# Kernel optimization log

Hardware: AMD Instinct MI355X
Metric: run time of the kernel (lower is better)

The kernel has to match this reference:

```python
import jax, jax.numpy as jnp
import numpy as np

NUM_EVENT, EVENT_DIM = 6, 32
NUM_WORD, WORD_DIM = 100000, 128
NUM_SKU, SKU_DIM = 500000, 128
NUM_CAT, CAT_DIM = 10000, 64
NUM_PRICE, PRICE_DIM = 100, 32
NUM_URL, URL_DIM = 200000, 128
HIDDEN = 512
B, S, W = 256, 256, 12
PAD = 0


def _table(key, n, d):
    t = jax.random.normal(key, (n, d), dtype=jnp.float32) * 0.02
    return t.at[PAD].set(0.0)  # padding_idx row is zero


def setup_inputs() -> dict:
    key = jax.random.key(0)
    ks = jax.random.split(key, 20)
    inp = {
        "event_table": _table(ks[0], NUM_EVENT, EVENT_DIM),
        "word_table": _table(ks[1], NUM_WORD, WORD_DIM),
        "sku_table": _table(ks[2], NUM_SKU, SKU_DIM),
        "cat_table": _table(ks[3], NUM_CAT, CAT_DIM),
        "price_table": _table(ks[4], NUM_PRICE, PRICE_DIM),
        "url_table": _table(ks[5], NUM_URL, URL_DIM),
        # Linear weights, torch convention: y = x @ W.T + b
        "sku_w": jax.random.normal(ks[6], (HIDDEN, EVENT_DIM + SKU_DIM + CAT_DIM + PRICE_DIM + WORD_DIM), dtype=jnp.float32) * 0.02,
        "sku_b": jnp.zeros((HIDDEN,), dtype=jnp.float32),
        "url_w": jax.random.normal(ks[7], (HIDDEN, URL_DIM + EVENT_DIM), dtype=jnp.float32) * 0.02,
        "url_b": jnp.zeros((HIDDEN,), dtype=jnp.float32),
        "query_w": jax.random.normal(ks[8], (HIDDEN, EVENT_DIM + WORD_DIM), dtype=jnp.float32) * 0.02,
        "query_b": jnp.zeros((HIDDEN,), dtype=jnp.float32),
        "event_type": jax.random.randint(ks[9], (B, S), 0, NUM_EVENT, dtype=jnp.int32),
        "sku_id": jax.random.randint(ks[10], (B, S), 0, NUM_SKU, dtype=jnp.int32),
        "url_id": jax.random.randint(ks[11], (B, S), 0, NUM_URL, dtype=jnp.int32),
        "cat_id": jax.random.randint(ks[12], (B, S), 0, NUM_CAT, dtype=jnp.int32),
        "price_id": jax.random.randint(ks[13], (B, S), 0, NUM_PRICE, dtype=jnp.int32),
        "word_id": jax.random.randint(ks[14], (B, S, W), 0, NUM_WORD, dtype=jnp.int32),
    }
    return inp


def _linear_relu(x, w, b):
    return jax.nn.relu(jnp.einsum("bsi,hi->bsh", x, w) + b)


def reference(event_table, word_table, sku_table, cat_table, price_table, url_table,
              sku_w, sku_b, url_w, url_b, query_w, query_b,
              event_type, sku_id, url_id, cat_id, price_id, word_id):
    # padding mask: 1.0 where event_type == PAD_IDX
    src_padding_mask = (event_type == PAD).astype(jnp.float32)

    event_emb = event_table[event_type]                 # [B,S,E]
    word_emb = word_table[word_id].mean(axis=-2)        # [B,S,Wd] (WordEmbedding avg)

    # SKU branch (event types 1,2,3): concat(event, sku, cat, price, word)
    sku_in = jnp.concatenate([event_emb, sku_table[sku_id], cat_table[cat_id],
                              price_table[price_id], word_emb], axis=-1)
    sku_out = _linear_relu(sku_in, sku_w, sku_b)        # [B,S,H]

    # URL branch (event type 4): concat(url, event)  -- note order in UrlEmbedding
    url_in = jnp.concatenate([url_table[url_id], event_emb], axis=-1)
    url_out = _linear_relu(url_in, url_w, url_b)

    # Query branch (event type 5): concat(event, word)
    query_in = jnp.concatenate([event_emb, word_emb], axis=-1)
    query_out = _linear_relu(query_in, query_w, query_b)

    is_sku = ((event_type >= 1) & (event_type <= 3))[..., None]
    is_url = (event_type == 4)[..., None]
    is_query = (event_type == 5)[..., None]

    seq_emb = (jnp.where(is_sku, sku_out, 0.0)
               + jnp.where(is_url, url_out, 0.0)
               + jnp.where(is_query, query_out, 0.0))   # PAD positions stay zero
    return seq_emb, src_padding_mask
```

## Files before the change

### kernel.cpp

```cpp
#include <hip/hip_runtime.h>
#include <hip/hip_bf16.h>
#if !__has_builtin(__builtin_amdgcn_cvt_pk_fp8_f32) || !__has_builtin(__builtin_amdgcn_cvt_pk_f32_fp8)
#include <hip/hip_fp8.h>
#endif

#define CUR_OFF   0
#define SLOT_OFF  1024
#define POS_OFF   263168
#define WSKU_OFF  1049600
#define WURL_OFF  1246208
#define WQRY_OFF  1377280
#define WF8_OFF   2097152
#define XS_OFF    16777216
#define XU_OFF    50331648
#define XQ_OFF    68157440

#define NPOS      65536
#define OUT_MASK  33554432
#define F8_SCALE  64.0f
#define INV4096   (1.0f / 4096.0f)

typedef __attribute__((ext_vector_type(4))) float f32x4;
typedef __attribute__((ext_vector_type(2))) float f32x2;
typedef __attribute__((ext_vector_type(2))) unsigned int u32x2;

__device__ __forceinline__ unsigned short f2bf(float x) {
    unsigned int u = __float_as_uint(x);
    return (unsigned short)((u + 0x7fffu + ((u >> 16) & 1u)) >> 16);
}
__device__ __forceinline__ float2 ld2(const float* p) {
    return *reinterpret_cast<const float2*>(p);
}

__device__ __forceinline__ unsigned int pk2_f8(float a, float b) {
#if __has_builtin(__builtin_amdgcn_cvt_pk_fp8_f32)
    return __builtin_amdgcn_cvt_pk_fp8_f32(a, b, 0u, false);
#else
    __hip_fp8_e4m3 fa(a), fb(b);
    return (unsigned int)fa.__x | ((unsigned int)fb.__x << 8);
#endif
}
__device__ __forceinline__ unsigned int pk4_f8(float a, float b, float c, float d) {
#if __has_builtin(__builtin_amdgcn_cvt_pk_fp8_f32)
    unsigned int v = 0;
    v = __builtin_amdgcn_cvt_pk_fp8_f32(a, b, v, false);
    v = __builtin_amdgcn_cvt_pk_fp8_f32(c, d, v, true);
    return v;
#else
    return pk2_f8(a, b) | (pk2_f8(c, d) << 16);
#endif
}
__device__ __forceinline__ float2 upk2_f8(unsigned int u) {
#if __has_builtin(__builtin_amdgcn_cvt_pk_f32_fp8)
    f32x2 r = __builtin_amdgcn_cvt_pk_f32_fp8(u, false);
    return make_float2(r.x, r.y);
#else
    __hip_fp8_e4m3 fa, fb;
    fa.__x = (unsigned char)(u & 0xff);
    fb.__x = (unsigned char)((u >> 8) & 0xff);
    return make_float2((float)fa, (float)fb);
#endif
}
__device__ __forceinline__ void st_f8x2(unsigned char* d, float a, float b) {
    *reinterpret_cast<unsigned short*>(d) = (unsigned short)(pk2_f8(a, b) & 0xffffu);
}

#define AS1(p) ((const __attribute__((address_space(1))) void*)(p))
#define AS3(p) ((__attribute__((address_space(3))) void*)(p))

__global__ __launch_bounds__(256) void prep_k(const float* __restrict__ sw,
                                              const float* __restrict__ uw,
                                              const float* __restrict__ qw,
                                              const float* __restrict__ word_t,
                                              char* ws) {
    const int b = blockIdx.x, t = threadIdx.x;
    if (b < 6250) {
        size_t i = ((size_t)b * 256 + t) * 8;
        f32x4 v0 = *reinterpret_cast<const f32x4*>(word_t + i);
        f32x4 v1 = *reinterpret_cast<const f32x4*>(word_t + i + 4);
        u32x2 pk;
        pk.x = pk4_f8(v0.x * F8_SCALE, v0.y * F8_SCALE, v0.z * F8_SCALE, v0.w * F8_SCALE);
        pk.y = pk4_f8(v1.x * F8_SCALE, v1.y * F8_SCALE, v1.z * F8_SCALE, v1.w * F8_SCALE);
        *reinterpret_cast<u32x2*>((unsigned char*)(ws + WF8_OFF) + i) = pk;
        return;
    }
    int tt = (b - 6250) * 256 + t;
    if (tt < 3) ((int*)(ws + CUR_OFF))[tt] = 0;
    if (tt < 196608) {
        ((unsigned char*)(ws + WSKU_OFF))[tt] =
            (unsigned char)(pk2_f8(sw[tt] * F8_SCALE, 0.f) & 0xffu);
    } else if (tt < 327680) {
        int i = tt - 196608; int n = i >> 8, k = i & 255;
        ((unsigned char*)(ws + WURL_OFF))[i] = (k < 160)
            ? (unsigned char)(pk2_f8(uw[n * 160 + k] * F8_SCALE, 0.f) & 0xffu) : 0;
    } else {
        int i = tt - 327680; int n = i >> 8, k = i & 255;
        ((unsigned char*)(ws + WQRY_OFF))[i] = (k < 160)
            ? (unsigned char)(pk2_f8(qw[n * 160 + k] * F8_SCALE, 0.f) & 0xffu) : 0;
    }
}

__global__ __launch_bounds__(256) void alloc_k(const int* __restrict__ et_a,
                                               float* __restrict__ out, char* ws) {
    __shared__ int s_wcnt[4][3];
    __shared__ int s_base[3];
    __shared__ int s_woff[4][3];
    const int t = threadIdx.x, lane = t & 63, wid = t >> 6;
    int p = blockIdx.x * 256 + t;
    int et = et_a[p];
    int br = (et >= 1 && et <= 3) ? 0 : (et == 4 ? 1 : (et == 5 ? 2 : -1));
    unsigned long long m0 = __ballot(br == 0);
    unsigned long long m1 = __ballot(br == 1);
    unsigned long long m2 = __ballot(br == 2);
    if (lane == 0) {
        s_wcnt[wid][0] = (int)__popcll(m0);
        s_wcnt[wid][1] = (int)__popcll(m1);
        s_wcnt[wid][2] = (int)__popcll(m2);
    }
    __syncthreads();
    if (t < 3) {
        int c0 = s_wcnt[0][t], c1 = s_wcnt[1][t], c2 = s_wcnt[2][t], c3 = s_wcnt[3][t];
        int tot = c0 + c1 + c2 + c3;
        s_base[t] = tot ? atomicAdd(&((int*)(ws + CUR_OFF))[t], tot) : 0;
        s_woff[0][t] = 0; s_woff[1][t] = c0; s_woff[2][t] = c0 + c1; s_woff[3][t] = c0 + c1 + c2;
    }
    __syncthreads();
    unsigned long long lt = (1ull << lane) - 1ull;
    int slot = -1;
    if (br == 0)      slot = s_base[0] + s_woff[wid][0] + (int)__popcll(m0 & lt);
    else if (br == 1) slot = s_base[1] + s_woff[wid][1] + (int)__popcll(m1 & lt);
    else if (br == 2) slot = s_base[2] + s_woff[wid][2] + (int)__popcll(m2 & lt);
    ((int*)(ws + SLOT_OFF))[p] = slot;
    if (slot >= 0) ((int*)(ws + POS_OFF))[br * NPOS + slot] = p;
    __builtin_nontemporal_store((et == 0) ? 1.0f : 0.0f, &out[OUT_MASK + p]);
}

__device__ __forceinline__ float2 wsum_f8(const unsigned char* __restrict__ wt8,
                                          const int* __restrict__ wids, int lane) {
    float sx = 0.f, sy = 0.f;
    #pragma unroll
    for (int k = 0; k < 12; ++k) {
        unsigned int u = *reinterpret_cast<const unsigned short*>(
            wt8 + (size_t)wids[k] * 128 + 2 * lane);
        float2 v = upk2_f8(u);
        sx += v.x; sy += v.y;
    }
    const float inv = 1.0f / 12.0f;
    return make_float2(sx * inv, sy * inv);
}

__global__ __launch_bounds__(256) void build_k(
    const float* __restrict__ ev_t,
    const float* __restrict__ sku_t,  const float* __restrict__ cat_t,
    const float* __restrict__ price_t,const float* __restrict__ url_t,
    const int* __restrict__ et_a,     const int* __restrict__ sku_id,
    const int* __restrict__ url_id,   const int* __restrict__ cat_id,
    const int* __restrict__ price_id, const int* __restrict__ word_id,
    float* __restrict__ out, char* ws)
{
    const int t = threadIdx.x, lane = t & 63, wid = t >> 6;
    const int p = blockIdx.x * 4 + wid;
    const int et = et_a[p];
    if (et == 0) {
        f32x4 z = {0.f, 0.f, 0.f, 0.f};
        float* orow = out + (size_t)p * 512;
        __builtin_nontemporal_store(z, reinterpret_cast<f32x4*>(&orow[lane * 8]));
        __builtin_nontemporal_store(z, reinterpret_cast<f32x4*>(&orow[lane * 8 + 4]));
        return;
    }
    const int slot = ((const int*)(ws + SLOT_OFF))[p];
    const unsigned char* wf8 = (const unsigned char*)(ws + WF8_OFF);
    const float* evr = ev_t + et * 32;
    if (et <= 3) {
        unsigned char* X = (unsigned char*)(ws + XS_OFF) + (size_t)slot * 384;
        if (lane < 16) { float2 e = ld2(evr + 2 * lane);
                         st_f8x2(X + 2 * lane, e.x * F8_SCALE, e.y * F8_SCALE); }
        const float* sr = sku_t + (size_t)sku_id[p] * 128;
        { float2 s = ld2(sr + 2 * lane);
          st_f8x2(X + 32 + 2 * lane, s.x * F8_SCALE, s.y * F8_SCALE); }
        if (lane < 32) { const float* cr = cat_t + (size_t)cat_id[p] * 64;
                         float2 c = ld2(cr + 2 * lane);
                         st_f8x2(X + 160 + 2 * lane, c.x * F8_SCALE, c.y * F8_SCALE); }
        if (lane < 16) { const float* pr = price_t + (size_t)price_id[p] * 32;
                         float2 v = ld2(pr + 2 * lane);
                         st_f8x2(X + 224 + 2 * lane, v.x * F8_SCALE, v.y * F8_SCALE); }
        float2 w = wsum_f8(wf8, word_id + (size_t)p * 12, lane);
        st_f8x2(X + 256 + 2 * lane, w.x, w.y);
    } else if (et == 4) {
        unsigned char* X = (unsigned char*)(ws + XU_OFF) + (size_t)slot * 256;
        const float* ur = url_t + (size_t)url_id[p] * 128;
        { float2 u = ld2(ur + 2 * lane);
          st_f8x2(X + 2 * lane, u.x * F8_SCALE, u.y * F8_SCALE); }
        if (lane < 16) { float2 e = ld2(evr + 2 * lane);
                         st_f8x2(X + 128 + 2 * lane, e.x * F8_SCALE, e.y * F8_SCALE); }
        if (lane < 48) *reinterpret_cast<unsigned short*>(X + 160 + 2 * lane) = 0;
    } else {
        unsigned char* X = (unsigned char*)(ws + XQ_OFF) + (size_t)slot * 256;
        if (lane < 16) { float2 e = ld2(evr + 2 * lane);
                         st_f8x2(X + 2 * lane, e.x * F8_SCALE, e.y * F8_SCALE); }
        float2 w = wsum_f8(wf8, word_id + (size_t)p * 12, lane);
        st_f8x2(X + 32 + 2 * lane, w.x, w.y);
        if (lane < 48) *reinterpret_cast<unsigned short*>(X + 160 + 2 * lane) = 0;
    }
}

__global__ __launch_bounds__(256, 2) void gemm_all_k(
    const char* __restrict__ ws_c, const float* __restrict__ sku_b,
    const float* __restrict__ url_b, const float* __restrict__ qry_b,
    float* __restrict__ out)
{
    const int z = blockIdx.z;
    const int count = ((const int*)(ws_c + CUR_OFF))[z];
    const int nmt = (count + 127) >> 7;
    const int nwg = nmt * 4;
    const int orig = blockIdx.x;
    if (orig >= nwg) return;
    const int q8 = nwg >> 3, r8 = nwg & 7;
    const int xcd = orig & 7, idx = orig >> 3;
    const int wg = (xcd < r8 ? xcd * (q8 + 1) : r8 * (q8 + 1) + (xcd - r8) * q8) + idx;
    const int mt = wg >> 2;
    const int row0 = mt * 128;
    const int nc0  = (wg & 3) * 128;

    const char* arena; const char* Wb; const float* bias; const int* posm;
    int astride, nkt;
    if (z == 0) { arena = ws_c + XS_OFF; Wb = ws_c + WSKU_OFF; bias = sku_b;
                  posm = (const int*)(ws_c + POS_OFF);          astride = 384; nkt = 3; }
    else if (z == 1) { arena = ws_c + XU_OFF; Wb = ws_c + WURL_OFF; bias = url_b;
                  posm = (const int*)(ws_c + POS_OFF) + NPOS;   astride = 256; nkt = 2; }
    else       { arena = ws_c + XQ_OFF; Wb = ws_c + WQRY_OFF; bias = qry_b;
                  posm = (const int*)(ws_c + POS_OFF) + 2*NPOS; astride = 256; nkt = 2; }

    __shared__ char lds[2][2][16384];

    const int t = threadIdx.x;
    const int lane = t & 63;
    const int wid  = t >> 6;
    const int wr = wid >> 1, wc = wid & 1;
    const int r = lane & 15, q = lane >> 4;

    auto stage = [&](int buf, int kt) {
        #pragma unroll
        for (int i = 0; i < 4; ++i) {
            int row = i * 32 + (t >> 3);
            int sb  = (t & 7) ^ (row & 7);
            const char* ga = arena + (size_t)(row0 + row) * astride + kt * 128 + sb * 16;
            __builtin_amdgcn_global_load_lds(AS1(ga), AS3(&lds[buf][0][i * 4096 + t * 16]), 16, 0, 0);
            const char* gb = Wb + (size_t)(nc0 + row) * astride + kt * 128 + sb * 16;
            __builtin_amdgcn_global_load_lds(AS1(gb), AS3(&lds[buf][1][i * 4096 + t * 16]), 16, 0, 0);
        }
    };

    f32x4 acc[4][4];
    #pragma unroll
    for (int m = 0; m < 4; ++m)
        #pragma unroll
        for (int n = 0; n < 4; ++n)
            acc[m][n] = (f32x4){0.f, 0.f, 0.f, 0.f};

    stage(0, 0);
    __syncthreads();
    int cur = 0;
    for (int kt = 0; kt < nkt; ++kt) {
        if (kt + 1 < nkt) stage(cur ^ 1, kt + 1);
        #pragma unroll
        for (int kk = 0; kk < 4; ++kk) {
            const int u  = kk * 2 + (q >> 1);
            const int wo = (q & 1) * 8;
            long af[4], bfr[4];
            #pragma unroll
            for (int m = 0; m < 4; ++m) {
                int arow = wr * 64 + m * 16 + r;
                af[m] = *reinterpret_cast<const long*>(
                    &lds[cur][0][arow * 128 + ((u ^ (arow & 7)) << 4) + wo]);
            }
            #pragma unroll
            for (int n = 0; n < 4; ++n) {
                int brow = wc * 64 + n * 16 + r;
                bfr[n] = *reinterpret_cast<const long*>(
                    &lds[cur][1][brow * 128 + ((u ^ (brow & 7)) << 4) + wo]);
            }
            #pragma unroll
            for (int m = 0; m < 4; ++m)
                #pragma unroll
                for (int n = 0; n < 4; ++n)
                    acc[m][n] = __builtin_amdgcn_mfma_f32_16x16x32_fp8_fp8(af[m], bfr[n], acc[m][n], 0, 0, 0);
        }
        __syncthreads();
        cur ^= 1;
    }

    float bv[4];
    #pragma unroll
    for (int n = 0; n < 4; ++n) bv[n] = bias[nc0 + wc * 64 + n * 16 + r];
    #pragma unroll
    for (int m = 0; m < 4; ++m) {
        #pragma unroll
        for (int j = 0; j < 4; ++j) {
            int rl = wr * 64 + m * 16 + q * 4 + j;
            int gr = row0 + rl;
            if (gr < count) {
                int pos = posm[gr];
                float* orow = out + (size_t)pos * 512 + nc0 + wc * 64;
                #pragma unroll
                for (int n = 0; n < 4; ++n)
                    __builtin_nontemporal_store(
                        fmaxf(acc[m][n][j] * INV4096 + bv[n], 0.f), &orow[n * 16 + r]);
            }
        }
    }
}

extern "C" void kernel_launch(void* const* d_in, const int* in_sizes, int n_in,
                              void* d_out, int out_size, void* d_ws, size_t ws_size,
                              hipStream_t stream) {
    const float* ev_t    = (const float*)d_in[0];
    const float* word_t  = (const float*)d_in[1];
    const float* sku_t   = (const float*)d_in[2];
    const float* cat_t   = (const float*)d_in[3];
    const float* price_t = (const float*)d_in[4];
    const float* url_t   = (const float*)d_in[5];
    const float* sku_w   = (const float*)d_in[6];
    const float* sku_b   = (const float*)d_in[7];
    const float* url_w   = (const float*)d_in[8];
    const float* url_b   = (const float*)d_in[9];
    const float* query_w = (const float*)d_in[10];
    const float* query_b = (const float*)d_in[11];
    const int* event_type = (const int*)d_in[12];
    const int* sku_id     = (const int*)d_in[13];
    const int* url_id     = (const int*)d_in[14];
    const int* cat_id     = (const int*)d_in[15];
    const int* price_id   = (const int*)d_in[16];
    const int* word_id    = (const int*)d_in[17];

    char*  ws  = (char*)d_ws;
    float* out = (float*)d_out;

    prep_k<<<8042, 256, 0, stream>>>(sku_w, url_w, query_w, word_t, ws);
    alloc_k<<<256, 256, 0, stream>>>(event_type, out, ws);
    build_k<<<16384, 256, 0, stream>>>(ev_t, sku_t, cat_t, price_t, url_t,
                                       event_type, sku_id, url_id, cat_id, price_id,
                                       word_id, out, ws);
    dim3 gg(2048, 1, 3);
    gemm_all_k<<<gg, 256, 0, stream>>>(ws, sku_b, url_b, query_b, out);
}
```

Baseline: 86.64 us.

## Shrink URL/query K padding from 256 to 192 with half-width second K tile

The URL and query branches have K=160. They were padded to 256, so two full 128-wide K tiles were staged and multiplied. This change pads them to 192 instead, and the second K tile now uses a 64-wide staging path with its own swizzle and half the MFMA steps. The goal is to cut redundant fp8 MFMA work and the memory traffic for the zero padding in two of the three GEMM branches, as well as the workspace writes. The cost is an extra branch and layout variant in the GEMM inner loop, plus new prep indexing that uses division and modulo by 192.

```diff
diff --git a/kernel.cpp b/kernel.cpp
--- a/kernel.cpp
+++ b/kernel.cpp
@@ -9,7 +9,7 @@
 #define POS_OFF   263168
 #define WSKU_OFF  1049600
 #define WURL_OFF  1246208
-#define WQRY_OFF  1377280
+#define WQRY_OFF  1344512
 #define WF8_OFF   2097152
 #define XS_OFF    16777216
 #define XU_OFF    50331648
@@ -24,10 +24,6 @@
 typedef __attribute__((ext_vector_type(2))) float f32x2;
 typedef __attribute__((ext_vector_type(2))) unsigned int u32x2;
 
-__device__ __forceinline__ unsigned short f2bf(float x) {
-    unsigned int u = __float_as_uint(x);
-    return (unsigned short)((u + 0x7fffu + ((u >> 16) & 1u)) >> 16);
-}
 __device__ __forceinline__ float2 ld2(const float* p) {
     return *reinterpret_cast<const float2*>(p);
 }
@@ -89,12 +85,12 @@
     if (tt < 196608) {
         ((unsigned char*)(ws + WSKU_OFF))[tt] =
             (unsigned char)(pk2_f8(sw[tt] * F8_SCALE, 0.f) & 0xffu);
-    } else if (tt < 327680) {
-        int i = tt - 196608; int n = i >> 8, k = i & 255;
+    } else if (tt < 294912) {
+        int i = tt - 196608; int n = i / 192, k = i % 192;
         ((unsigned char*)(ws + WURL_OFF))[i] = (k < 160)
             ? (unsigned char)(pk2_f8(uw[n * 160 + k] * F8_SCALE, 0.f) & 0xffu) : 0;
     } else {
-        int i = tt - 327680; int n = i >> 8, k = i & 255;
+        int i = tt - 294912; int n = i / 192, k = i % 192;
         ((unsigned char*)(ws + WQRY_OFF))[i] = (k < 160)
             ? (unsigned char)(pk2_f8(qw[n * 160 + k] * F8_SCALE, 0.f) & 0xffu) : 0;
     }
@@ -187,20 +183,20 @@
         float2 w = wsum_f8(wf8, word_id + (size_t)p * 12, lane);
         st_f8x2(X + 256 + 2 * lane, w.x, w.y);
     } else if (et == 4) {
-        unsigned char* X = (unsigned char*)(ws + XU_OFF) + (size_t)slot * 256;
+        unsigned char* X = (unsigned char*)(ws + XU_OFF) + (size_t)slot * 192;
         const float* ur = url_t + (size_t)url_id[p] * 128;
         { float2 u = ld2(ur + 2 * lane);
           st_f8x2(X + 2 * lane, u.x * F8_SCALE, u.y * F8_SCALE); }
         if (lane < 16) { float2 e = ld2(evr + 2 * lane);
                          st_f8x2(X + 128 + 2 * lane, e.x * F8_SCALE, e.y * F8_SCALE); }
-        if (lane < 48) *reinterpret_cast<unsigned short*>(X + 160 + 2 * lane) = 0;
+        if (lane >= 48) *reinterpret_cast<unsigned short*>(X + 160 + 2 * (lane - 48)) = 0;
     } else {
-        unsigned char* X = (unsigned char*)(ws + XQ_OFF) + (size_t)slot * 256;
+        unsigned char* X = (unsigned char*)(ws + XQ_OFF) + (size_t)slot * 192;
         if (lane < 16) { float2 e = ld2(evr + 2 * lane);
                          st_f8x2(X + 2 * lane, e.x * F8_SCALE, e.y * F8_SCALE); }
         float2 w = wsum_f8(wf8, word_id + (size_t)p * 12, lane);
         st_f8x2(X + 32 + 2 * lane, w.x, w.y);
-        if (lane < 48) *reinterpret_cast<unsigned short*>(X + 160 + 2 * lane) = 0;
+        if (lane >= 48) *reinterpret_cast<unsigned short*>(X + 160 + 2 * (lane - 48)) = 0;
     }
 }
 
@@ -227,9 +223,9 @@
     if (z == 0) { arena = ws_c + XS_OFF; Wb = ws_c + WSKU_OFF; bias = sku_b;
                   posm = (const int*)(ws_c + POS_OFF);          astride = 384; nkt = 3; }
     else if (z == 1) { arena = ws_c + XU_OFF; Wb = ws_c + WURL_OFF; bias = url_b;
-                  posm = (const int*)(ws_c + POS_OFF) + NPOS;   astride = 256; nkt = 2; }
+                  posm = (const int*)(ws_c + POS_OFF) + NPOS;   astride = 192; nkt = 2; }
     else       { arena = ws_c + XQ_OFF; Wb = ws_c + WQRY_OFF; bias = qry_b;
-                  posm = (const int*)(ws_c + POS_OFF) + 2*NPOS; astride = 256; nkt = 2; }
+                  posm = (const int*)(ws_c + POS_OFF) + 2*NPOS; astride = 192; nkt = 2; }
 
     __shared__ char lds[2][2][16384];
 
@@ -239,15 +235,27 @@
     const int wr = wid >> 1, wc = wid & 1;
     const int r = lane & 15, q = lane >> 4;
 
-    auto stage = [&](int buf, int kt) {
-        #pragma unroll
-        for (int i = 0; i < 4; ++i) {
-            int row = i * 32 + (t >> 3);
-            int sb  = (t & 7) ^ (row & 7);
-            const char* ga = arena + (size_t)(row0 + row) * astride + kt * 128 + sb * 16;
-            __builtin_amdgcn_global_load_lds(AS1(ga), AS3(&lds[buf][0][i * 4096 + t * 16]), 16, 0, 0);
-            const char* gb = Wb + (size_t)(nc0 + row) * astride + kt * 128 + sb * 16;
-            __builtin_amdgcn_global_load_lds(AS1(gb), AS3(&lds[buf][1][i * 4096 + t * 16]), 16, 0, 0);
+    auto stage = [&](int buf, int koff, bool full) {
+        if (full) {
+            #pragma unroll
+            for (int i = 0; i < 4; ++i) {
+                int row = i * 32 + (t >> 3);
+                int sb  = (t & 7) ^ (row & 7);
+                const char* ga = arena + (size_t)(row0 + row) * astride + koff + sb * 16;
+                __builtin_amdgcn_global_load_lds(AS1(ga), AS3(&lds[buf][0][i * 4096 + t * 16]), 16, 0, 0);
+                const char* gb = Wb + (size_t)(nc0 + row) * astride + koff + sb * 16;
+                __builtin_amdgcn_global_load_lds(AS1(gb), AS3(&lds[buf][1][i * 4096 + t * 16]), 16, 0, 0);
+            }
+        } else {
+            #pragma unroll
+            for (int i = 0; i < 2; ++i) {
+                int row = i * 64 + (t >> 2);
+                int sb  = (t & 3) ^ (row & 3);
+                const char* ga = arena + (size_t)(row0 + row) * astride + koff + sb * 16;
+                __builtin_amdgcn_global_load_lds(AS1(ga), AS3(&lds[buf][0][i * 4096 + t * 16]), 16, 0, 0);
+                const char* gb = Wb + (size_t)(nc0 + row) * astride + koff + sb * 16;
+                __builtin_amdgcn_global_load_lds(AS1(gb), AS3(&lds[buf][1][i * 4096 + t * 16]), 16, 0, 0);
+            }
         }
     };
 
@@ -258,33 +266,60 @@
         for (int n = 0; n < 4; ++n)
             acc[m][n] = (f32x4){0.f, 0.f, 0.f, 0.f};
 
-    stage(0, 0);
+    stage(0, 0, true);
     __syncthreads();
     int cur = 0;
     for (int kt = 0; kt < nkt; ++kt) {
-        if (kt + 1 < nkt) stage(cur ^ 1, kt + 1);
-        #pragma unroll
-        for (int kk = 0; kk < 4; ++kk) {
-            const int u  = kk * 2 + (q >> 1);
-            const int wo = (q & 1) * 8;
-            long af[4], bfr[4];
+        const bool full = (z == 0) || (kt == 0);
+        if (kt + 1 < nkt) stage(cur ^ 1, (kt + 1) * 128, (z == 0));
+        if (full) {
             #pragma unroll
-            for (int m = 0; m < 4; ++m) {
-                int arow = wr * 64 + m * 16 + r;
-                af[m] = *reinterpret_cast<const long*>(
-                    &lds[cur][0][arow * 128 + ((u ^ (arow & 7)) << 4) + wo]);
-            }
+            for (int kk = 0; kk < 4; ++kk) {
+                const int u  = kk * 2 + (q >> 1);
+                const int wo = (q & 1) * 8;
+                long af[4], bfr[4];
+                #pragma unroll
+                for (int m = 0; m < 4; ++m) {
+                    int arow = wr * 64 + m * 16 + r;
+                    af[m] = *reinterpret_cast<const long*>(
+                        &lds[cur][0][arow * 128 + ((u ^ (arow & 7)) << 4) + wo]);
+                }
+                #pragma unroll
+                for (int n = 0; n < 4; ++n) {
+                    int brow = wc * 64 + n * 16 + r;
+                    bfr[n] = *reinterpret_cast<const long*>(
+                        &lds[cur][1][brow * 128 + ((u ^ (brow & 7)) << 4) + wo]);
+                }
+                #pragma unroll
+                for (int m = 0; m < 4; ++m)
+                    #pragma unroll
+                    for (int n = 0; n < 4; ++n)
+                        acc[m][n] = __builtin_amdgcn_mfma_f32_16x16x32_fp8_fp8(af[m], bfr[n], acc[m][n], 0, 0, 0);
+            }
+        } else {
             #pragma unroll
-            for (int n = 0; n < 4; ++n) {
-                int brow = wc * 64 + n * 16 + r;
-                bfr[n] = *reinterpret_cast<const long*>(
-                    &lds[cur][1][brow * 128 + ((u ^ (brow & 7)) << 4) + wo]);
-            }
-            #pragma unroll
-            for (int m = 0; m < 4; ++m)
-                #pragma unroll
-                for (int n = 0; n < 4; ++n)
-                    acc[m][n] = __builtin_amdgcn_mfma_f32_16x16x32_fp8_fp8(af[m], bfr[n], acc[m][n], 0, 0, 0);
+            for (int kk = 0; kk < 2; ++kk) {
+                const int u  = kk * 2 + (q >> 1);
+                const int wo = (q & 1) * 8;
+                long af[4], bfr[4];
+                #pragma unroll
+                for (int m = 0; m < 4; ++m) {
+                    int arow = wr * 64 + m * 16 + r;
+                    af[m] = *reinterpret_cast<const long*>(
+                        &lds[cur][0][arow * 64 + ((u ^ (arow & 3)) << 4) + wo]);
+                }
+                #pragma unroll
+                for (int n = 0; n < 4; ++n) {
+                    int brow = wc * 64 + n * 16 + r;
+                    bfr[n] = *reinterpret_cast<const long*>(
+                        &lds[cur][1][brow * 64 + ((u ^ (brow & 3)) << 4) + wo]);
+                }
+                #pragma unroll
+                for (int m = 0; m < 4; ++m)
+                    #pragma unroll
+                    for (int n = 0; n < 4; ++n)
+                        acc[m][n] = __builtin_amdgcn_mfma_f32_16x16x32_fp8_fp8(af[m], bfr[n], acc[m][n], 0, 0, 0);
+            }
         }
         __syncthreads();
         cur ^= 1;
@@ -336,7 +371,7 @@
     char*  ws  = (char*)d_ws;
     float* out = (float*)d_out;
 
-    prep_k<<<8042, 256, 0, stream>>>(sku_w, url_w, query_w, word_t, ws);
+    prep_k<<<7786, 256, 0, stream>>>(sku_w, url_w, query_w, word_t, ws);
     alloc_k<<<256, 256, 0, stream>>>(event_type, out, ws);
     build_k<<<16384, 256, 0, stream>>>(ev_t, sku_t, cat_t, price_t, url_t,
                                        event_type, sku_id, url_id, cat_id, price_id,
```

After: 86.76 us. No clear change (+0.1%).
